# Kernel tuning notes

Measured on AMD Instinct MI355X. Metric: run time of the kernel, lower is better.

## Reference

```python
import jax, jax.numpy as jnp
import numpy as np

K_TOP = 2        # experts_per_tok
E_MLP = 8        # num_mlp_experts


def setup_inputs() -> dict:
    key = jax.random.key(0)
    ks = jax.random.split(key, 6)
    B, T, C, H, E_ve, V = 2, 2048, 1024, 2048, 2, 32000
    return {
        "x": jax.random.normal(ks[0], (B, T, C), dtype=jnp.float32),
        "token_ids": jax.random.randint(ks[1], (B, T), 0, V, dtype=jnp.int32),
        "w_up": jax.random.normal(ks[2], (E_MLP, H, C), dtype=jnp.float32) * 0.02,
        "w_down": jax.random.normal(ks[3], (E_MLP, C, H), dtype=jnp.float32) * 0.02,
        "router_w": jax.random.normal(ks[4], (E_MLP + E_ve, C), dtype=jnp.float32) * 0.02,
        "router_bias": jnp.zeros((E_MLP + E_ve,), dtype=jnp.float32),
        "ve_tables": jax.random.normal(ks[5], (E_ve, V, C), dtype=jnp.float32) * 0.02,
    }


def reference(x, token_ids, w_up, w_down, router_w, router_bias, ve_tables):
    B, T, C = x.shape
    N = B * T
    E_total = router_w.shape[0]
    x_flat = x.reshape(N, C)

    # Sigmoid router with aux-loss-free bias (DeepSeekV3 style): select top-k on
    # biased scores, gate with unbiased sigmoid scores normalized over the top-k.
    scores = jax.nn.sigmoid(x_flat @ router_w.T)              # (N, E_total)
    _, top_idx = jax.lax.top_k(scores + router_bias, K_TOP)   # (N, k)
    top_w = jnp.take_along_axis(scores, top_idx, axis=1)      # (N, k)
    top_w = top_w / jnp.sum(top_w, axis=1, keepdims=True)

    rows = jnp.arange(N)[:, None]
    sparse_w = jnp.zeros((N, E_total), dtype=x.dtype).at[rows, top_idx].set(top_w)

    # Dense all-expert FFN (relu^2 activation), then mask by routing weights.
    hidden = jnp.einsum('nc,ehc->enh', x_flat, w_up)          # (E_mlp, N, H)
    hidden = jnp.square(jax.nn.relu(hidden))
    mlp_out = jnp.einsum('enh,ech->enc', hidden, w_down)      # (E_mlp, N, C)
    mlp_contrib = jnp.einsum('enc,ne->nc', mlp_out, sparse_w[:, :E_MLP])

    # VE experts: shared embedding lookups, (E_ve, N, C).
    ve_out = ve_tables[:, token_ids.reshape(N), :]
    ve_contrib = jnp.einsum('enc,ne->nc', ve_out, sparse_w[:, E_MLP:])

    return (mlp_contrib + ve_contrib).reshape(B, T, C)
```

## Files before the change

### kernel.cpp

```cpp
#include <hip/hip_runtime.h>
#include <hip/hip_bf16.h>
#include <stdint.h>

#define N_TOK 4096
#define C_DIM 1024
#define H_DIM 2048
#define V_DIM 32000
#define NE_MLP 8
#define NE_TOT 10

typedef __attribute__((ext_vector_type(8))) short bf16x8;
typedef __attribute__((ext_vector_type(4))) short bf16x4;
typedef __attribute__((ext_vector_type(4))) float f32x4;

#define BM 128
#define BN 128
#define HKE 32
#define HALF_ELEMS (128 * 32)

__device__ __forceinline__ void gload16(const void* g, void* l) {
    __builtin_amdgcn_global_load_lds(
        (const __attribute__((address_space(1))) void*)g,
        (__attribute__((address_space(3))) void*)l,
        16, 0, 0);
}

__device__ __forceinline__ unsigned short bf16bits(float v) {
    __hip_bfloat16 h = __float2bfloat16(v);
    return *reinterpret_cast<unsigned short*>(&h);
}

#define CVT_W (NE_MLP * H_DIM * C_DIM / 4)
__global__ void __launch_bounds__(256) cvt_kernel(
    const float* __restrict__ wu, const float* __restrict__ wd,
    __hip_bfloat16* __restrict__ wub, __hip_bfloat16* __restrict__ wdb)
{
    const int i = blockIdx.x * 256 + threadIdx.x;
    const float* src;
    __hip_bfloat16* dst;
    int j;
    if (i < CVT_W) { src = wu; dst = wub; j = i; }
    else           { src = wd; dst = wdb; j = i - CVT_W; }
    f32x4 v = reinterpret_cast<const f32x4*>(src)[j];
    bf16x4 b;
    b.x = (short)bf16bits(v.x); b.y = (short)bf16bits(v.y);
    b.z = (short)bf16bits(v.z); b.w = (short)bf16bits(v.w);
    reinterpret_cast<bf16x4*>(dst)[j] = b;
}

__global__ void __launch_bounds__(256) router_kernel(
    const float* __restrict__ x, const float* __restrict__ rw,
    const float* __restrict__ rb, __hip_bfloat16* __restrict__ xb,
    int* __restrict__ tok_list, float* __restrict__ wlist,
    float* __restrict__ vw, int* __restrict__ cnt)
{
    const int lane = threadIdx.x & 63;
    const int n = blockIdx.x * 4 + (threadIdx.x >> 6);
    const f32x4* xr  = reinterpret_cast<const f32x4*>(x + (size_t)n * C_DIM);
    const f32x4* rw4 = reinterpret_cast<const f32x4*>(rw);
    bf16x4* xbr = reinterpret_cast<bf16x4*>(xb + (size_t)n * C_DIM);

    float acc[NE_TOT];
    #pragma unroll
    for (int e = 0; e < NE_TOT; ++e) acc[e] = 0.f;

    #pragma unroll
    for (int kk = 0; kk < C_DIM / 256; ++kk) {
        f32x4 xv = xr[kk * 64 + lane];
        bf16x4 xbv;
        xbv.x = (short)bf16bits(xv.x); xbv.y = (short)bf16bits(xv.y);
        xbv.z = (short)bf16bits(xv.z); xbv.w = (short)bf16bits(xv.w);
        xbr[kk * 64 + lane] = xbv;
        #pragma unroll
        for (int e = 0; e < NE_TOT; ++e) {
            f32x4 wv = rw4[e * (C_DIM / 4) + kk * 64 + lane];
            acc[e] += xv.x * wv.x + xv.y * wv.y + xv.z * wv.z + xv.w * wv.w;
        }
    }
    #pragma unroll
    for (int e = 0; e < NE_TOT; ++e) {
        for (int m = 32; m > 0; m >>= 1) acc[e] += __shfl_xor(acc[e], m, 64);
    }

    if (lane == 0) {
        float s[NE_TOT], sb[NE_TOT];
        #pragma unroll
        for (int e = 0; e < NE_TOT; ++e) {
            s[e]  = 1.f / (1.f + expf(-acc[e]));
            sb[e] = s[e] + rb[e];
        }
        int i0 = 0;
        #pragma unroll
        for (int e = 1; e < NE_TOT; ++e) if (sb[e] > sb[i0]) i0 = e;
        int i1 = (i0 == 0) ? 1 : 0;
        #pragma unroll
        for (int e = 0; e < NE_TOT; ++e)
            if (e != i0 && sb[e] > sb[i1]) i1 = e;

        float w0 = s[i0], w1 = s[i1];
        float inv = 1.f / (w0 + w1);
        w0 *= inv; w1 *= inv;

        float wv0 = 0.f, wv1 = 0.f;
        int   idx[2] = {i0, i1};
        float wt[2]  = {w0, w1};
        #pragma unroll
        for (int k = 0; k < 2; ++k) {
            if (idx[k] < NE_MLP) {
                int p = atomicAdd(&cnt[idx[k]], 1);
                tok_list[idx[k] * N_TOK + p] = n;
                wlist[idx[k] * N_TOK + p] = wt[k];
            } else {
                if (idx[k] == NE_MLP) wv0 = wt[k]; else wv1 = wt[k];
            }
        }
        vw[n * 2 + 0] = wv0;
        vw[n * 2 + 1] = wv1;
    }
}

__global__ void __launch_bounds__(256) ve_kernel(
    const int* __restrict__ token_ids, const float* __restrict__ vt,
    const float* __restrict__ vw, float* __restrict__ out)
{
    const int n = blockIdx.x;
    const int c = threadIdx.x;
    const int t = token_ids[n];
    const float w0 = vw[n * 2 + 0];
    const float w1 = vw[n * 2 + 1];
    f32x4 v = {0.f, 0.f, 0.f, 0.f};
    if (w0 != 0.f)
        v += w0 * reinterpret_cast<const f32x4*>(vt + (size_t)t * C_DIM)[c];
    if (w1 != 0.f)
        v += w1 * reinterpret_cast<const f32x4*>(vt + ((size_t)V_DIM + t) * C_DIM)[c];
    reinterpret_cast<f32x4*>(out + (size_t)n * C_DIM)[c] = v;
}

__global__ void __launch_bounds__(256) up_kernel(
    const __hip_bfloat16* __restrict__ xb, const __hip_bfloat16* __restrict__ wub,
    const int* __restrict__ tok_list, const int* __restrict__ cnt,
    __hip_bfloat16* __restrict__ hidden)
{
    const int lid = (blockIdx.z * 32 + blockIdx.y) * 16 + blockIdx.x;
    const int s   = (lid & 7) * 512 + (lid >> 3);
    const int bx = s & 15, by = (s >> 4) & 31, bz = s >> 9;

    const int e = bz;
    const int count = cnt[e];
    const int m0 = by * BM;
    if (m0 >= count) return;
    const int n0 = bx * BN;

    __shared__ __hip_bfloat16 lA[2 * HALF_ELEMS];
    __shared__ __hip_bfloat16 lB[2 * HALF_ELEMS];

    const int tid  = threadIdx.x;
    const int lane = tid & 63;
    const int wv   = tid >> 6;
    const int wm = (wv >> 1) * 64;
    const int wn = (wv & 1) * 64;

    const __hip_bfloat16* ga[2];
    const __hip_bfloat16* gb[2];
    __hip_bfloat16* la[2];
    __hip_bfloat16* lb[2];
    const __hip_bfloat16* wB = wub + (size_t)e * H_DIM * C_DIM;
    #pragma unroll
    for (int t = 0; t < 2; ++t) {
        const int srow = (wv + 4 * t) * 16 + (lane >> 2);
        int r = m0 + srow;
        const int tok = tok_list[e * N_TOK + (r < count ? r : count - 1)];
        ga[t] = xb + (size_t)tok * C_DIM + (lane & 3) * 8;
        gb[t] = wB + (size_t)(n0 + srow) * C_DIM + (lane & 3) * 8;
        la[t] = lA + (wv + 4 * t) * 512;
        lb[t] = lB + (wv + 4 * t) * 512;
    }

    f32x4 acc[4][4];
    #pragma unroll
    for (int i = 0; i < 4; ++i)
        #pragma unroll
        for (int j = 0; j < 4; ++j)
            acc[i][j] = (f32x4){0.f, 0.f, 0.f, 0.f};

    const int fm  = lane & 15;
    const int fkb = (lane >> 4) * 8;

    for (int k0 = 0; k0 < C_DIM; k0 += 2 * HKE) {
        __syncthreads();
        #pragma unroll
        for (int h = 0; h < 2; ++h) {
            #pragma unroll
            for (int t = 0; t < 2; ++t) {
                gload16(ga[t] + h * HKE, la[t] + h * HALF_ELEMS);
                gload16(gb[t] + h * HKE, lb[t] + h * HALF_ELEMS);
            }
        }
        #pragma unroll
        for (int t = 0; t < 2; ++t) { ga[t] += 2 * HKE; gb[t] += 2 * HKE; }
        __syncthreads();
        #pragma unroll
        for (int h = 0; h < 2; ++h) {
            bf16x8 af[4], bfr[4];
            #pragma unroll
            for (int i = 0; i < 4; ++i) {
                af[i]  = *reinterpret_cast<const bf16x8*>(lA + h * HALF_ELEMS + (wm + i * 16 + fm) * HKE + fkb);
                bfr[i] = *reinterpret_cast<const bf16x8*>(lB + h * HALF_ELEMS + (wn + i * 16 + fm) * HKE + fkb);
            }
            #pragma unroll
            for (int i = 0; i < 4; ++i)
                #pragma unroll
                for (int j = 0; j < 4; ++j)
                    acc[i][j] = __builtin_amdgcn_mfma_f32_16x16x32_bf16(af[i], bfr[j], acc[i][j], 0, 0, 0);
        }
    }

    const int fr = (lane >> 4) * 4;
    #pragma unroll
    for (int i = 0; i < 4; ++i) {
        #pragma unroll
        for (int r = 0; r < 4; ++r) {
            const int gr = m0 + wm + i * 16 + fr + r;
            const bool ok = gr < count;
            unsigned int pk[4];
            #pragma unroll
            for (int j = 0; j < 4; ++j) {
                float v = acc[i][j][r];
                v = v > 0.f ? v * v : 0.f;
                unsigned short b = bf16bits(v);
                int other = __shfl_xor((int)b, 1, 64);
                pk[j] = (unsigned)b | ((unsigned)other << 16);
            }
            if (ok && !(lane & 1)) {
                __hip_bfloat16* hrow = hidden + (size_t)(e * N_TOK + gr) * H_DIM + n0 + wn + fm;
                #pragma unroll
                for (int j = 0; j < 4; ++j)
                    *reinterpret_cast<unsigned int*>(hrow + j * 16) = pk[j];
            }
        }
    }
}

__global__ void __launch_bounds__(256) down_kernel(
    const __hip_bfloat16* __restrict__ hidden, const __hip_bfloat16* __restrict__ wdb,
    const int* __restrict__ tok_list, const float* __restrict__ wlist,
    const int* __restrict__ cnt, float* __restrict__ out)
{
    const int lid = (blockIdx.z * 32 + blockIdx.y) * 8 + blockIdx.x;
    const int s   = (lid & 7) * 512 + (lid >> 3);
    const int bx = s & 7, by = (s >> 3) & 31, bz = s >> 8;

    const int e  = bz >> 1;
    const int kh = bz & 1;
    const int count = cnt[e];
    const int m0 = by * BM;
    if (m0 >= count) return;
    const int n0 = bx * BN;
    const int kbase = kh * (H_DIM / 2);

    __shared__ __hip_bfloat16 lA[2 * HALF_ELEMS];
    __shared__ __hip_bfloat16 lB[2 * HALF_ELEMS];

    const int tid  = threadIdx.x;
    const int lane = tid & 63;
    const int wv   = tid >> 6;
    const int wm = (wv >> 1) * 64;
    const int wn = (wv & 1) * 64;

    const __hip_bfloat16* ga[2];
    const __hip_bfloat16* gb[2];
    __hip_bfloat16* la[2];
    __hip_bfloat16* lb[2];
    const __hip_bfloat16* wB = wdb + (size_t)e * C_DIM * H_DIM;
    #pragma unroll
    for (int t = 0; t < 2; ++t) {
        const int srow = (wv + 4 * t) * 16 + (lane >> 2);
        int r = m0 + srow;
        const int arow = e * N_TOK + (r < count ? r : count - 1);
        ga[t] = hidden + (size_t)arow * H_DIM + kbase + (lane & 3) * 8;
        gb[t] = wB + (size_t)(n0 + srow) * H_DIM + kbase + (lane & 3) * 8;
        la[t] = lA + (wv + 4 * t) * 512;
        lb[t] = lB + (wv + 4 * t) * 512;
    }

    f32x4 acc[4][4];
    #pragma unroll
    for (int i = 0; i < 4; ++i)
        #pragma unroll
        for (int j = 0; j < 4; ++j)
            acc[i][j] = (f32x4){0.f, 0.f, 0.f, 0.f};

    const int fm  = lane & 15;
    const int fkb = (lane >> 4) * 8;

    for (int k0 = 0; k0 < H_DIM / 2; k0 += 2 * HKE) {
        __syncthreads();
        #pragma unroll
        for (int h = 0; h < 2; ++h) {
            #pragma unroll
            for (int t = 0; t < 2; ++t) {
                gload16(ga[t] + h * HKE, la[t] + h * HALF_ELEMS);
                gload16(gb[t] + h * HKE, lb[t] + h * HALF_ELEMS);
            }
        }
        #pragma unroll
        for (int t = 0; t < 2; ++t) { ga[t] += 2 * HKE; gb[t] += 2 * HKE; }
        __syncthreads();
        #pragma unroll
        for (int h = 0; h < 2; ++h) {
            bf16x8 af[4], bfr[4];
            #pragma unroll
            for (int i = 0; i < 4; ++i) {
                af[i]  = *reinterpret_cast<const bf16x8*>(lA + h * HALF_ELEMS + (wm + i * 16 + fm) * HKE + fkb);
                bfr[i] = *reinterpret_cast<const bf16x8*>(lB + h * HALF_ELEMS + (wn + i * 16 + fm) * HKE + fkb);
            }
            #pragma unroll
            for (int i = 0; i < 4; ++i)
                #pragma unroll
                for (int j = 0; j < 4; ++j)
                    acc[i][j] = __builtin_amdgcn_mfma_f32_16x16x32_bf16(af[i], bfr[j], acc[i][j], 0, 0, 0);
        }
    }

    const int fr = (lane >> 4) * 4;
    #pragma unroll
    for (int i = 0; i < 4; ++i) {
        #pragma unroll
        for (int r = 0; r < 4; ++r) {
            const int gr = m0 + wm + i * 16 + fr + r;
            if (gr < count) {
                const int   tok = tok_list[e * N_TOK + gr];
                const float w   = wlist[e * N_TOK + gr];
                float* orow = out + (size_t)tok * C_DIM + n0 + wn + fm;
                #pragma unroll
                for (int j = 0; j < 4; ++j)
                    __hip_atomic_fetch_add(orow + j * 16, w * acc[i][j][r],
                                           __ATOMIC_RELAXED, __HIP_MEMORY_SCOPE_AGENT);
            }
        }
    }
}

extern "C" void kernel_launch(void* const* d_in, const int* in_sizes, int n_in,
                              void* d_out, int out_size, void* d_ws, size_t ws_size,
                              hipStream_t stream)
{
    const float* x         = (const float*)d_in[0];
    const int*   token_ids = (const int*)  d_in[1];
    const float* w_up      = (const float*)d_in[2];
    const float* w_down    = (const float*)d_in[3];
    const float* router_w  = (const float*)d_in[4];
    const float* router_b  = (const float*)d_in[5];
    const float* ve_tables = (const float*)d_in[6];
    float* out = (float*)d_out;

    char* ws = (char*)d_ws;
    size_t off = 0;
    __hip_bfloat16* hidden  = (__hip_bfloat16*)(ws + off); off += (size_t)NE_MLP * N_TOK * H_DIM * 2;
    __hip_bfloat16* xb      = (__hip_bfloat16*)(ws + off); off += (size_t)N_TOK * C_DIM * 2;
    __hip_bfloat16* wub     = (__hip_bfloat16*)(ws + off); off += (size_t)NE_MLP * H_DIM * C_DIM * 2;
    __hip_bfloat16* wdb     = (__hip_bfloat16*)(ws + off); off += (size_t)NE_MLP * C_DIM * H_DIM * 2;
    int*   tok_list = (int*)  (ws + off); off += (size_t)NE_MLP * N_TOK * 4;
    float* wlist    = (float*)(ws + off); off += (size_t)NE_MLP * N_TOK * 4;
    float* vw       = (float*)(ws + off); off += (size_t)N_TOK * 2 * 4;
    int*   cnt      = (int*)  (ws + off); off += 64;

    hipMemsetAsync(cnt, 0, NE_MLP * sizeof(int), stream);

    router_kernel<<<N_TOK / 4, 256, 0, stream>>>(x, router_w, router_b, xb,
                                                 tok_list, wlist, vw, cnt);
    cvt_kernel<<<2 * CVT_W / 256, 256, 0, stream>>>(w_up, w_down, wub, wdb);
    ve_kernel<<<N_TOK, 256, 0, stream>>>(token_ids, ve_tables, vw, out);
    up_kernel<<<dim3(H_DIM / BN, N_TOK / BM, NE_MLP), 256, 0, stream>>>(
        xb, wub, tok_list, cnt, hidden);
    down_kernel<<<dim3(C_DIM / BN, N_TOK / BM, NE_MLP * 2), 256, 0, stream>>>(
        hidden, wdb, tok_list, wlist, cnt, out);
}
```

Baseline: 596.3 us.

## Fuse VE lookup into router and replace down split-K with narrower N tiles

The value-embedding gather and weighted write move into the router kernel. The router broadcasts the VE gate weights across the wavefront, so the separate ve_kernel launch and the vw round-trip through memory go away. The down-projection drops its two-way split over H and uses 128x64 output tiles over the full H range instead. This halves the number of atomic adds into the output and keeps the block count the same. In exchange, each block runs a longer K loop and reuses the A tile less per load, since its B tile is half as wide.

```diff
diff --git a/kernel.cpp b/kernel.cpp
--- a/kernel.cpp
+++ b/kernel.cpp
@@ -15,8 +15,10 @@
 
 #define BM 128
 #define BN 128
+#define BND 64
 #define HKE 32
 #define HALF_ELEMS (128 * 32)
+#define HALF_B (64 * 32)
 
 __device__ __forceinline__ void gload16(const void* g, void* l) {
     __builtin_amdgcn_global_load_lds(
@@ -50,9 +52,10 @@
 
 __global__ void __launch_bounds__(256) router_kernel(
     const float* __restrict__ x, const float* __restrict__ rw,
-    const float* __restrict__ rb, __hip_bfloat16* __restrict__ xb,
+    const float* __restrict__ rb, const int* __restrict__ token_ids,
+    const float* __restrict__ vt, __hip_bfloat16* __restrict__ xb,
     int* __restrict__ tok_list, float* __restrict__ wlist,
-    float* __restrict__ vw, int* __restrict__ cnt)
+    int* __restrict__ cnt, float* __restrict__ out)
 {
     const int lane = threadIdx.x & 63;
     const int n = blockIdx.x * 4 + (threadIdx.x >> 6);
@@ -82,6 +85,7 @@
         for (int m = 32; m > 0; m >>= 1) acc[e] += __shfl_xor(acc[e], m, 64);
     }
 
+    float wv0 = 0.f, wv1 = 0.f;
     if (lane == 0) {
         float s[NE_TOT], sb[NE_TOT];
         #pragma unroll
@@ -101,7 +105,6 @@
         float inv = 1.f / (w0 + w1);
         w0 *= inv; w1 *= inv;
 
-        float wv0 = 0.f, wv1 = 0.f;
         int   idx[2] = {i0, i1};
         float wt[2]  = {w0, w1};
         #pragma unroll
@@ -114,26 +117,21 @@
                 if (idx[k] == NE_MLP) wv0 = wt[k]; else wv1 = wt[k];
             }
         }
-        vw[n * 2 + 0] = wv0;
-        vw[n * 2 + 1] = wv1;
-    }
-}
-
-__global__ void __launch_bounds__(256) ve_kernel(
-    const int* __restrict__ token_ids, const float* __restrict__ vt,
-    const float* __restrict__ vw, float* __restrict__ out)
-{
-    const int n = blockIdx.x;
-    const int c = threadIdx.x;
+    }
+    wv0 = __shfl(wv0, 0, 64);
+    wv1 = __shfl(wv1, 0, 64);
     const int t = token_ids[n];
-    const float w0 = vw[n * 2 + 0];
-    const float w1 = vw[n * 2 + 1];
-    f32x4 v = {0.f, 0.f, 0.f, 0.f};
-    if (w0 != 0.f)
-        v += w0 * reinterpret_cast<const f32x4*>(vt + (size_t)t * C_DIM)[c];
-    if (w1 != 0.f)
-        v += w1 * reinterpret_cast<const f32x4*>(vt + ((size_t)V_DIM + t) * C_DIM)[c];
-    reinterpret_cast<f32x4*>(out + (size_t)n * C_DIM)[c] = v;
+    const f32x4* v0 = reinterpret_cast<const f32x4*>(vt + (size_t)t * C_DIM);
+    const f32x4* v1 = reinterpret_cast<const f32x4*>(vt + ((size_t)V_DIM + t) * C_DIM);
+    f32x4* orow = reinterpret_cast<f32x4*>(out + (size_t)n * C_DIM);
+    #pragma unroll
+    for (int q = 0; q < 4; ++q) {
+        const int c = q * 64 + lane;
+        f32x4 v = {0.f, 0.f, 0.f, 0.f};
+        if (wv0 != 0.f) v += wv0 * v0[c];
+        if (wv1 != 0.f) v += wv1 * v1[c];
+        orow[c] = v;
+    }
 }
 
 __global__ void __launch_bounds__(256) up_kernel(
@@ -246,78 +244,76 @@
     const int* __restrict__ tok_list, const float* __restrict__ wlist,
     const int* __restrict__ cnt, float* __restrict__ out)
 {
-    const int lid = (blockIdx.z * 32 + blockIdx.y) * 8 + blockIdx.x;
+    const int lid = (blockIdx.z * 32 + blockIdx.y) * 16 + blockIdx.x;
     const int s   = (lid & 7) * 512 + (lid >> 3);
-    const int bx = s & 7, by = (s >> 3) & 31, bz = s >> 8;
-
-    const int e  = bz >> 1;
-    const int kh = bz & 1;
+    const int bx = s & 15, by = (s >> 4) & 31, bz = s >> 9;
+
+    const int e = bz;
     const int count = cnt[e];
     const int m0 = by * BM;
     if (m0 >= count) return;
-    const int n0 = bx * BN;
-    const int kbase = kh * (H_DIM / 2);
+    const int n0 = bx * BND;
 
     __shared__ __hip_bfloat16 lA[2 * HALF_ELEMS];
-    __shared__ __hip_bfloat16 lB[2 * HALF_ELEMS];
+    __shared__ __hip_bfloat16 lB[2 * HALF_B];
 
     const int tid  = threadIdx.x;
     const int lane = tid & 63;
     const int wv   = tid >> 6;
     const int wm = (wv >> 1) * 64;
-    const int wn = (wv & 1) * 64;
+    const int wn = (wv & 1) * 32;
 
     const __hip_bfloat16* ga[2];
-    const __hip_bfloat16* gb[2];
     __hip_bfloat16* la[2];
-    __hip_bfloat16* lb[2];
-    const __hip_bfloat16* wB = wdb + (size_t)e * C_DIM * H_DIM;
     #pragma unroll
     for (int t = 0; t < 2; ++t) {
         const int srow = (wv + 4 * t) * 16 + (lane >> 2);
         int r = m0 + srow;
         const int arow = e * N_TOK + (r < count ? r : count - 1);
-        ga[t] = hidden + (size_t)arow * H_DIM + kbase + (lane & 3) * 8;
-        gb[t] = wB + (size_t)(n0 + srow) * H_DIM + kbase + (lane & 3) * 8;
+        ga[t] = hidden + (size_t)arow * H_DIM + (lane & 3) * 8;
         la[t] = lA + (wv + 4 * t) * 512;
-        lb[t] = lB + (wv + 4 * t) * 512;
-    }
-
-    f32x4 acc[4][4];
+    }
+    const int srowB = wv * 16 + (lane >> 2);
+    const __hip_bfloat16* gb = wdb + (size_t)e * C_DIM * H_DIM
+                             + (size_t)(n0 + srowB) * H_DIM + (lane & 3) * 8;
+    __hip_bfloat16* lb = lB + wv * 512;
+
+    f32x4 acc[4][2];
     #pragma unroll
     for (int i = 0; i < 4; ++i)
         #pragma unroll
-        for (int j = 0; j < 4; ++j)
+        for (int j = 0; j < 2; ++j)
             acc[i][j] = (f32x4){0.f, 0.f, 0.f, 0.f};
 
     const int fm  = lane & 15;
     const int fkb = (lane >> 4) * 8;
 
-    for (int k0 = 0; k0 < H_DIM / 2; k0 += 2 * HKE) {
+    for (int k0 = 0; k0 < H_DIM; k0 += 2 * HKE) {
         __syncthreads();
         #pragma unroll
         for (int h = 0; h < 2; ++h) {
             #pragma unroll
-            for (int t = 0; t < 2; ++t) {
+            for (int t = 0; t < 2; ++t)
                 gload16(ga[t] + h * HKE, la[t] + h * HALF_ELEMS);
-                gload16(gb[t] + h * HKE, lb[t] + h * HALF_ELEMS);
-            }
-        }
-        #pragma unroll
-        for (int t = 0; t < 2; ++t) { ga[t] += 2 * HKE; gb[t] += 2 * HKE; }
+            gload16(gb + h * HKE, lb + h * HALF_B);
+        }
+        #pragma unroll
+        for (int t = 0; t < 2; ++t) ga[t] += 2 * HKE;
+        gb += 2 * HKE;
         __syncthreads();
         #pragma unroll
         for (int h = 0; h < 2; ++h) {
-            bf16x8 af[4], bfr[4];
-            #pragma unroll
-            for (int i = 0; i < 4; ++i) {
+            bf16x8 af[4], bfr[2];
+            #pragma unroll
+            for (int i = 0; i < 4; ++i)
                 af[i]  = *reinterpret_cast<const bf16x8*>(lA + h * HALF_ELEMS + (wm + i * 16 + fm) * HKE + fkb);
-                bfr[i] = *reinterpret_cast<const bf16x8*>(lB + h * HALF_ELEMS + (wn + i * 16 + fm) * HKE + fkb);
-            }
+            #pragma unroll
+            for (int j = 0; j < 2; ++j)
+                bfr[j] = *reinterpret_cast<const bf16x8*>(lB + h * HALF_B + (wn + j * 16 + fm) * HKE + fkb);
             #pragma unroll
             for (int i = 0; i < 4; ++i)
                 #pragma unroll
-                for (int j = 0; j < 4; ++j)
+                for (int j = 0; j < 2; ++j)
                     acc[i][j] = __builtin_amdgcn_mfma_f32_16x16x32_bf16(af[i], bfr[j], acc[i][j], 0, 0, 0);
         }
     }
@@ -333,7 +329,7 @@
                 const float w   = wlist[e * N_TOK + gr];
                 float* orow = out + (size_t)tok * C_DIM + n0 + wn + fm;
                 #pragma unroll
-                for (int j = 0; j < 4; ++j)
+                for (int j = 0; j < 2; ++j)
                     __hip_atomic_fetch_add(orow + j * 16, w * acc[i][j][r],
                                            __ATOMIC_RELAXED, __HIP_MEMORY_SCOPE_AGENT);
             }
@@ -362,17 +358,16 @@
     __hip_bfloat16* wdb     = (__hip_bfloat16*)(ws + off); off += (size_t)NE_MLP * C_DIM * H_DIM * 2;
     int*   tok_list = (int*)  (ws + off); off += (size_t)NE_MLP * N_TOK * 4;
     float* wlist    = (float*)(ws + off); off += (size_t)NE_MLP * N_TOK * 4;
-    float* vw       = (float*)(ws + off); off += (size_t)N_TOK * 2 * 4;
     int*   cnt      = (int*)  (ws + off); off += 64;
 
     hipMemsetAsync(cnt, 0, NE_MLP * sizeof(int), stream);
 
-    router_kernel<<<N_TOK / 4, 256, 0, stream>>>(x, router_w, router_b, xb,
-                                                 tok_list, wlist, vw, cnt);
+    router_kernel<<<N_TOK / 4, 256, 0, stream>>>(x, router_w, router_b,
+                                                 token_ids, ve_tables, xb,
+                                                 tok_list, wlist, cnt, out);
     cvt_kernel<<<2 * CVT_W / 256, 256, 0, stream>>>(w_up, w_down, wub, wdb);
-    ve_kernel<<<N_TOK, 256, 0, stream>>>(token_ids, ve_tables, vw, out);
     up_kernel<<<dim3(H_DIM / BN, N_TOK / BM, NE_MLP), 256, 0, stream>>>(
         xb, wub, tok_list, cnt, hidden);
-    down_kernel<<<dim3(C_DIM / BN, N_TOK / BM, NE_MLP * 2), 256, 0, stream>>>(
+    down_kernel<<<dim3(C_DIM / BND, N_TOK / BM, NE_MLP), 256, 0, stream>>>(
         hidden, wdb, tok_list, wlist, cnt, out);
 }
```

Result: faster. 583.0 us (-2.2%).
